# Kernel optimization log

Measured on AMD Instinct MI355X. Metric: run time of the kernel, lower is better.

Reference implementation:

```python
import jax, jax.numpy as jnp
import numpy as np

NUM = 5   # grid intervals
K = 3     # spline order


def make_grid(in_dim, num=NUM, k=K, lo=-1.0, hi=1.0):
    # pykan: linspace over [lo,hi] with num+1 knots, extended by k on each side
    g = np.linspace(lo, hi, num + 1)
    h = (g[-1] - g[0]) / num
    left = g[0] - h * np.arange(k, 0, -1)
    right = g[-1] + h * np.arange(1, k + 1)
    g = np.concatenate([left, g, right])  # (num + 2k + 1,)
    return jnp.asarray(np.broadcast_to(g, (in_dim, g.shape[0])), dtype=jnp.float32)


def b_batch(x, grid, k=K):
    # x: (B, in), grid: (in, G) -> B-spline bases (B, in, G-k-1) via Cox-de Boor
    xe = x[:, :, None]                      # (B, in, 1)
    g = grid[None]                          # (1, in, G)
    B = ((xe >= g[:, :, :-1]) & (xe < g[:, :, 1:])).astype(x.dtype)
    for ki in range(1, k + 1):
        B = ((xe - g[:, :, :-(ki + 1)]) / (g[:, :, ki:-1] - g[:, :, :-(ki + 1)]) * B[:, :, :-1]
             + (g[:, :, ki + 1:] - xe) / (g[:, :, ki + 1:] - g[:, :, 1:-ki]) * B[:, :, 1:])
    return jnp.nan_to_num(B)


def kan_layer(x, grid, coef, scale_base, scale_sp, mask, k=K):
    # x: (B, in); coef: (in, out, num+k); scales/mask: (in, out)
    base = jax.nn.silu(x)                             # (B, in)
    Bsp = b_batch(x, grid, k)                         # (B, in, num+k)
    y = jnp.einsum('bik,iok->bio', Bsp, coef)         # spline curves (B, in, out)
    y = scale_base[None] * base[:, :, None] + scale_sp[None] * y
    y = mask[None] * y
    return jnp.sum(y, axis=1)                         # (B, out)


def setup_inputs() -> dict:
    key = jax.random.key(0)
    ks = jax.random.split(key, 10)
    B, IN, HID, OUT = 4096, 1024, 256, 128
    KC = NUM + K  # coef count per edge
    x = jax.random.normal(ks[0], (B, IN), dtype=jnp.float32)
    W1 = jax.random.normal(ks[1], (HID, IN), dtype=jnp.float32) / np.sqrt(IN)
    b1 = jnp.zeros((HID,), dtype=jnp.float32)
    grid1 = make_grid(HID)
    coef1 = jax.random.normal(ks[2], (HID, HID, KC), dtype=jnp.float32) * 0.1
    sb1 = jax.random.normal(ks[3], (HID, HID), dtype=jnp.float32) / np.sqrt(HID)
    sp1 = jnp.ones((HID, HID), dtype=jnp.float32) / np.sqrt(HID)
    mask1 = jnp.ones((HID, HID), dtype=jnp.float32)
    grid2 = make_grid(HID)
    coef2 = jax.random.normal(ks[4], (HID, OUT, KC), dtype=jnp.float32) * 0.1
    sb2 = jax.random.normal(ks[5], (HID, OUT), dtype=jnp.float32) / np.sqrt(HID)
    sp2 = jnp.ones((HID, OUT), dtype=jnp.float32) / np.sqrt(HID)
    mask2 = jnp.ones((HID, OUT), dtype=jnp.float32)
    return {"x": x, "W1": W1, "b1": b1,
            "grid1": grid1, "coef1": coef1, "sb1": sb1, "sp1": sp1, "mask1": mask1,
            "grid2": grid2, "coef2": coef2, "sb2": sb2, "sp2": sp2, "mask2": mask2}


def reference(x, W1, b1, grid1, coef1, sb1, sp1, mask1, grid2, coef2, sb2, sp2, mask2):
    h = x @ W1.T + b1                                  # fc1
    h = kan_layer(h, grid1, coef1, sb1, sp1, mask1)    # kanl1
    out = kan_layer(h, grid2, coef2, sb2, sp2, mask2)  # kanl2
    return out
```

## Files before the change

kernel.cpp:

```cpp
#include <hip/hip_runtime.h>
#include <math.h>

typedef unsigned short u16;
typedef u16 u16x4 __attribute__((ext_vector_type(4)));
typedef u16 u16x8 __attribute__((ext_vector_type(8)));
typedef float f32x4 __attribute__((ext_vector_type(4)));
typedef float f32x16 __attribute__((ext_vector_type(16)));
typedef __bf16 bf16x8 __attribute__((ext_vector_type(8)));

#define KC 8
#define K2L 2304

__device__ __forceinline__ u16 f2bf_rne(float f) {
  unsigned u = __float_as_uint(f);
  u += 0x7FFFu + ((u >> 16) & 1u);
  return (u16)(u >> 16);
}
__device__ __forceinline__ float bf2f(u16 h) {
  return __uint_as_float(((unsigned)h) << 16);
}

__device__ __forceinline__ void gload16(const u16* g, u16* l) {
  __builtin_amdgcn_global_load_lds(
      (const __attribute__((address_space(1))) unsigned*)g,
      (__attribute__((address_space(3))) unsigned*)l, 16, 0, 0);
}
template <int N>
__device__ __forceinline__ void vmwait() {
  if constexpr (N == 0)      asm volatile("s_waitcnt vmcnt(0)" ::: "memory");
  else if constexpr (N == 3) asm volatile("s_waitcnt vmcnt(3)" ::: "memory");
  else if constexpr (N == 4) asm volatile("s_waitcnt vmcnt(4)" ::: "memory");
  else if constexpr (N == 6) asm volatile("s_waitcnt vmcnt(6)" ::: "memory");
  else if constexpr (N == 8) asm volatile("s_waitcnt vmcnt(8)" ::: "memory");
  else static_assert(N == 0, "unsupported vmcnt literal");
}

__device__ __forceinline__ void split4(const float* X, u16* hi, u16* lo, int i) {
  f32x4 v = ((const f32x4*)X)[i];
  u16x4 h, l;
#pragma unroll
  for (int c = 0; c < 4; ++c) {
    u16 hb = f2bf_rne(v[c]);
    h[c] = hb;
    l[c] = f2bf_rne(v[c] - bf2f(hb));
  }
  ((u16x4*)hi)[i] = h;
  ((u16x4*)lo)[i] = l;
}
__device__ __forceinline__ void split4hi(const float* X, u16* hi, int i) {
  f32x4 v = ((const f32x4*)X)[i];
  u16x4 h;
#pragma unroll
  for (int c = 0; c < 4; ++c) h[c] = f2bf_rne(v[c]);
  ((u16x4*)hi)[i] = h;
}
__device__ __forceinline__ void wc_one(const float* coef, const float* sb, const float* sp,
                                       const float* mask, u16* W, int N, int idx) {
  int o = idx / K2L;
  int r = idx - o * K2L;
  int i = r / 9;
  int c = r - i * 9;
  int io = i * N + o;
  float m = mask[io];
  float v = (c == 0) ? m * sb[io] : m * sp[io] * coef[(size_t)io * KC + (c - 1)];
  W[idx] = f2bf_rne(v);
}

__global__ void prep_kernel(const float* __restrict__ x, const float* __restrict__ W1,
                            const float* __restrict__ coef1, const float* __restrict__ sb1,
                            const float* __restrict__ sp1, const float* __restrict__ mask1,
                            const float* __restrict__ coef2, const float* __restrict__ sb2,
                            const float* __restrict__ sp2, const float* __restrict__ mask2,
                            u16* __restrict__ xs_hi,
                            u16* __restrict__ w1_hi, u16* __restrict__ w1_lo,
                            u16* __restrict__ wc1, u16* __restrict__ wc2) {
  const int b = blockIdx.x, tid = threadIdx.x;
  if (b < 4096) {
    split4hi(x, xs_hi, b * 256 + tid);
  } else if (b < 4096 + 256) {
    split4(W1, w1_hi, w1_lo, (b - 4096) * 256 + tid);
  } else if (b < 4096 + 256 + 2304) {
    wc_one(coef1, sb1, sp1, mask1, wc1, 256, (b - 4352) * 256 + tid);
  } else {
    wc_one(coef2, sb2, sp2, mask2, wc2, 128, (b - 6656) * 256 + tid);
  }
}

struct Spl {
  float g[12];
  float d1[11], d2[10], d3[9];
};
__device__ __forceinline__ void spl_init(const float* __restrict__ grid, Spl& sp) {
#pragma unroll
  for (int j = 0; j < 12; ++j) sp.g[j] = grid[j];
#pragma unroll
  for (int j = 0; j < 11; ++j) sp.d1[j] = 1.0f / (sp.g[j + 1] - sp.g[j]);
#pragma unroll
  for (int j = 0; j < 10; ++j) sp.d2[j] = 1.0f / (sp.g[j + 2] - sp.g[j]);
#pragma unroll
  for (int j = 0; j < 9; ++j) sp.d3[j] = 1.0f / (sp.g[j + 3] - sp.g[j]);
}
__device__ __forceinline__ void expand_one(float v, const Spl& sp, u16* dst) {
  float Bv[11];
#pragma unroll
  for (int j = 0; j < 11; ++j) Bv[j] = (v >= sp.g[j] && v < sp.g[j + 1]) ? 1.0f : 0.0f;
#pragma unroll
  for (int j = 0; j < 10; ++j)
    Bv[j] = (v - sp.g[j]) * sp.d1[j] * Bv[j] + (sp.g[j + 2] - v) * sp.d1[j + 1] * Bv[j + 1];
#pragma unroll
  for (int j = 0; j < 9; ++j)
    Bv[j] = (v - sp.g[j]) * sp.d2[j] * Bv[j] + (sp.g[j + 3] - v) * sp.d2[j + 1] * Bv[j + 1];
#pragma unroll
  for (int j = 0; j < 8; ++j)
    Bv[j] = (v - sp.g[j]) * sp.d3[j] * Bv[j] + (sp.g[j + 4] - v) * sp.d3[j + 1] * Bv[j + 1];
  dst[0] = f2bf_rne(v / (1.0f + __expf(-v)));
#pragma unroll
  for (int k = 0; k < 8; ++k) dst[1 + k] = f2bf_rne(Bv[k]);
}

template <int NREG, int MQ, int NQ, int KG, bool EXPAND>
__global__ __launch_bounds__(512) void gemmW(
    const u16* __restrict__ A0, const u16* __restrict__ B0, const u16* __restrict__ B1,
    const float* __restrict__ bias, const float* __restrict__ grid,
    void* __restrict__ outv, int M, int N, int K, int nsteps) {
  static_assert(MQ * NQ * KG == 8, "8 waves");
  constexpr int BM = MQ * 32, BN = NQ * 32;
  constexpr int ASZ = BM * 128;
  constexpr int BUF_U16 = (BM + BN) * 128;
  constexpr int NCH = (BM + BN) * 16;
  constexpr int LPT = NCH / 512;
  constexpr int SPK = 8 / KG;
  __shared__ __align__(16) u16 smu[4 * BUF_U16];

  const int tid = threadIdx.x;
  const int lane = tid & 63;
  const int wid = tid >> 6;
  const int q = wid % (MQ * NQ);
  const int kg = wid / (MQ * NQ);
  const int mq = (NQ == 2) ? (q >> 1) : q;
  const int nq = (NQ == 2) ? (q & 1) : 0;

  const int nb = N / BN;
  const int nwg = (M / BM) * nb;
  const int bid = blockIdx.x;
  const int swz = (bid & 7) * (nwg >> 3) + (bid >> 3);
  const int tm = (swz / nb) * BM;
  const int tn = (swz % nb) * BN;

  const u16* pA0 = A0 + (size_t)tm * K;
  const u16* pB0 = B0 + (size_t)tn * K;
  const u16* pB1 = (NREG == 2) ? B1 + (size_t)tn * K : nullptr;

  int srcO[LPT];
  bool isA[LPT];
#pragma unroll
  for (int k = 0; k < LPT; ++k) {
    int c = tid + k * 512;
    bool a = c < BM * 16;
    int r = a ? (c >> 4) : ((c - BM * 16) >> 4);
    int sl = c & 15;
    isA[k] = a;
    srcO[k] = r * K + (((sl ^ (r & 15)) & 15) << 3);
  }

  const int lr = lane & 31;
  const int khf = lane >> 5;

  int offA[SPK], offB[SPK];
#pragma unroll
  for (int s = 0; s < SPK; ++s) {
    int slice = kg * SPK + s;
    int rowA = mq * 32 + lr;
    int rowB = nq * 32 + lr;
    offA[s] = rowA * 128 + ((((slice * 2 + khf) ^ (rowA & 15)) & 15) << 3);
    offB[s] = rowB * 128 + ((((slice * 2 + khf) ^ (rowB & 15)) & 15) << 3);
  }

  auto stage = [&](int buf, int step) {
    int kk;
    const u16 *Ab, *Bb;
    if constexpr (NREG == 2) {
      int reg = step >> 3;
      kk = (step & 7) << 7;
      Ab = pA0;
      Bb = (reg == 1) ? pB1 : pB0;
    } else {
      kk = step << 7;
      Ab = pA0;
      Bb = pB0;
    }
    u16* sb = smu + buf * BUF_U16;
#pragma unroll
    for (int k = 0; k < LPT; ++k)
      gload16((isA[k] ? Ab : Bb) + srcO[k] + kk, sb + (k * 512 + wid * 64) * 8);
  };

  f32x16 acc0 = {}, acc1 = {};
  stage(0, 0);
  stage(1, 1);
  for (int i = 0; i < nsteps; ++i) {
    if (i + 2 < nsteps) {
      stage((i + 2) & 3, i + 2);
      vmwait<2 * LPT>();
    } else if (i + 1 < nsteps) {
      vmwait<LPT>();
    } else {
      vmwait<0>();
    }
    __builtin_amdgcn_sched_barrier(0);
    __builtin_amdgcn_s_barrier();
    __builtin_amdgcn_sched_barrier(0);

    const u16* sb = smu + (i & 3) * BUF_U16;
    bf16x8 af[SPK], bfr[SPK];
#pragma unroll
    for (int s = 0; s < SPK; ++s) {
      af[s] = *(const bf16x8*)(sb + offA[s]);
      bfr[s] = *(const bf16x8*)(sb + ASZ + offB[s]);
    }
#pragma unroll
    for (int s = 0; s < SPK; ++s) {
      f32x16& ac = (s & 1) ? acc1 : acc0;
      ac = __builtin_amdgcn_mfma_f32_32x32x16_bf16(af[s], bfr[s], ac, 0, 0, 0);
    }
  }
  f32x16 accv = acc0 + acc1;

  const int rbase = 4 * khf;
  const int rowq = mq * 32, colq = nq * 32;

  float* Fr = (float*)smu;
  if constexpr (KG == 2) {
    __syncthreads();
    if (kg == 1) {
#pragma unroll
      for (int r = 0; r < 16; ++r) {
        int row = rowq + rbase + (r & 3) + 8 * (r >> 2);
        Fr[row * BN + colq + lr] = accv[r];
      }
    }
    __syncthreads();
    if (kg == 0) {
#pragma unroll
      for (int r = 0; r < 16; ++r) {
        int row = rowq + rbase + (r & 3) + 8 * (r >> 2);
        accv[r] += Fr[row * BN + colq + lr];
      }
    }
  } else {
    __syncthreads();
    if (kg >= 2) {
#pragma unroll
      for (int r = 0; r < 16; ++r) {
        int row = rowq + rbase + (r & 3) + 8 * (r >> 2);
        Fr[(kg - 2) * (BM * BN) + row * BN + colq + lr] = accv[r];
      }
    }
    __syncthreads();
    if (kg < 2) {
#pragma unroll
      for (int r = 0; r < 16; ++r) {
        int row = rowq + rbase + (r & 3) + 8 * (r >> 2);
        accv[r] += Fr[kg * (BM * BN) + row * BN + colq + lr];
      }
    }
    __syncthreads();
    if (kg == 1) {
#pragma unroll
      for (int r = 0; r < 16; ++r) {
        int row = rowq + rbase + (r & 3) + 8 * (r >> 2);
        Fr[row * BN + colq + lr] = accv[r];
      }
    }
    __syncthreads();
    if (kg == 0) {
#pragma unroll
      for (int r = 0; r < 16; ++r) {
        int row = rowq + rbase + (r & 3) + 8 * (r >> 2);
        accv[r] += Fr[row * BN + colq + lr];
      }
    }
  }

  if constexpr (EXPAND) {
    Spl sp;
    spl_init(grid, sp);
    __syncthreads();
    u16* Fl = smu;
    if (kg == 0) {
      int col = colq + lr;
      float bv = bias ? bias[tn + col] : 0.0f;
#pragma unroll
      for (int r = 0; r < 16; ++r) {
        int row = rowq + rbase + (r & 3) + 8 * (r >> 2);
        expand_one(accv[r] + bv, sp, Fl + (size_t)row * (BN * 9) + col * 9);
      }
    }
    __syncthreads();
    u16* Fout = (u16*)outv;
    constexpr int RB = BN * 9 / 8;
    constexpr int CH = BM * RB;
    const size_t fstride = (size_t)N * 9;
    for (int ch = tid; ch < CH; ch += 512) {
      int r = ch / RB, o = ch - r * RB;
      *(u16x8*)(Fout + (size_t)(tm + r) * fstride + (size_t)tn * 9 + o * 8) =
          *(const u16x8*)(Fl + (size_t)ch * 8);
    }
  } else {
    if (kg == 0) {
      float* Cp = (float*)outv;
      const int cbase = tn + colq + lr;
#pragma unroll
      for (int r = 0; r < 16; ++r) {
        int row = tm + rowq + rbase + (r & 3) + 8 * (r >> 2);
        Cp[(size_t)row * N + cbase] = accv[r];
      }
    }
  }
}

extern "C" void kernel_launch(void* const* d_in, const int* in_sizes, int n_in,
                              void* d_out, int out_size, void* d_ws, size_t ws_size,
                              hipStream_t stream) {
  (void)in_sizes; (void)n_in; (void)out_size; (void)ws_size;
  const float* x     = (const float*)d_in[0];
  const float* W1    = (const float*)d_in[1];
  const float* b1    = (const float*)d_in[2];
  const float* grid1 = (const float*)d_in[3];
  const float* coef1 = (const float*)d_in[4];
  const float* sb1   = (const float*)d_in[5];
  const float* sp1   = (const float*)d_in[6];
  const float* mask1 = (const float*)d_in[7];
  const float* grid2 = (const float*)d_in[8];
  const float* coef2 = (const float*)d_in[9];
  const float* sb2   = (const float*)d_in[10];
  const float* sp2   = (const float*)d_in[11];
  const float* mask2 = (const float*)d_in[12];
  float* outp = (float*)d_out;

  char* ws = (char*)d_ws;
  size_t off = 0;
  auto alloc = [&](size_t bytes) {
    char* p = ws + off;
    off += (bytes + 255) & ~(size_t)255;
    return (void*)p;
  };
  u16* xs_hi  = (u16*)alloc((size_t)4096 * 1024 * 2);
  u16* w1_hi  = (u16*)alloc((size_t)256 * 1024 * 2);
  u16* w1_lo  = (u16*)alloc((size_t)256 * 1024 * 2);
  u16* wc1    = (u16*)alloc((size_t)256 * K2L * 2);
  u16* wc2    = (u16*)alloc((size_t)128 * K2L * 2);
  u16* F1     = (u16*)alloc((size_t)4096 * K2L * 2);
  u16* F2     = (u16*)alloc((size_t)4096 * K2L * 2);

  prep_kernel<<<7808, 256, 0, stream>>>(x, W1, coef1, sb1, sp1, mask1,
                                        coef2, sb2, sp2, mask2,
                                        xs_hi, w1_hi, w1_lo, wc1, wc2);

  gemmW<2, 2, 2, 2, true><<<256, 512, 0, stream>>>(
      xs_hi, w1_hi, w1_lo, b1, grid1, F1, 4096, 256, 1024, 16);

  gemmW<1, 2, 2, 2, true><<<256, 512, 0, stream>>>(
      F1, wc1, nullptr, nullptr, grid2, F2, 4096, 256, 2304, 18);

  gemmW<1, 2, 1, 4, false><<<256, 512, 0, stream>>>(
      F2, wc2, nullptr, nullptr, nullptr, outp, 4096, 128, 2304, 18);
}
```

Before: 62.06 us.

## Drop W1 low-part split and share spline expansion across both K-groups

Removes the bf16 hi/lo split of W1, so the first GEMM runs only 8 K-steps against a single bf16 copy of W1 instead of 16 steps over two copies. It also changes the KG=2 reduction to a symmetric exchange so both K-group waves hold the full sum. Each group then expands half of the rows into B-spline features, splitting work that one group did alone before. This lowers the accuracy of fc1, since W1 now carries only bf16 precision, which could affect tolerance near spline knot boundaries.

```diff
diff --git a/kernel.cpp b/kernel.cpp
--- a/kernel.cpp
+++ b/kernel.cpp
@@ -15,9 +15,6 @@
   unsigned u = __float_as_uint(f);
   u += 0x7FFFu + ((u >> 16) & 1u);
   return (u16)(u >> 16);
-}
-__device__ __forceinline__ float bf2f(u16 h) {
-  return __uint_as_float(((unsigned)h) << 16);
 }
 
 __device__ __forceinline__ void gload16(const u16* g, u16* l) {
@@ -35,18 +32,6 @@
   else static_assert(N == 0, "unsupported vmcnt literal");
 }
 
-__device__ __forceinline__ void split4(const float* X, u16* hi, u16* lo, int i) {
-  f32x4 v = ((const f32x4*)X)[i];
-  u16x4 h, l;
-#pragma unroll
-  for (int c = 0; c < 4; ++c) {
-    u16 hb = f2bf_rne(v[c]);
-    h[c] = hb;
-    l[c] = f2bf_rne(v[c] - bf2f(hb));
-  }
-  ((u16x4*)hi)[i] = h;
-  ((u16x4*)lo)[i] = l;
-}
 __device__ __forceinline__ void split4hi(const float* X, u16* hi, int i) {
   f32x4 v = ((const f32x4*)X)[i];
   u16x4 h;
@@ -71,14 +56,13 @@
                             const float* __restrict__ sp1, const float* __restrict__ mask1,
                             const float* __restrict__ coef2, const float* __restrict__ sb2,
                             const float* __restrict__ sp2, const float* __restrict__ mask2,
-                            u16* __restrict__ xs_hi,
-                            u16* __restrict__ w1_hi, u16* __restrict__ w1_lo,
+                            u16* __restrict__ xs_hi, u16* __restrict__ w1_hi,
                             u16* __restrict__ wc1, u16* __restrict__ wc2) {
   const int b = blockIdx.x, tid = threadIdx.x;
   if (b < 4096) {
     split4hi(x, xs_hi, b * 256 + tid);
   } else if (b < 4096 + 256) {
-    split4(W1, w1_hi, w1_lo, (b - 4096) * 256 + tid);
+    split4hi(W1, w1_hi, (b - 4096) * 256 + tid);
   } else if (b < 4096 + 256 + 2304) {
     wc_one(coef1, sb1, sp1, mask1, wc1, 256, (b - 4352) * 256 + tid);
   } else {
@@ -118,17 +102,16 @@
   for (int k = 0; k < 8; ++k) dst[1 + k] = f2bf_rne(Bv[k]);
 }
 
-template <int NREG, int MQ, int NQ, int KG, bool EXPAND>
+template <int MQ, int NQ, int KG, bool EXPAND>
 __global__ __launch_bounds__(512) void gemmW(
-    const u16* __restrict__ A0, const u16* __restrict__ B0, const u16* __restrict__ B1,
+    const u16* __restrict__ A0, const u16* __restrict__ B0,
     const float* __restrict__ bias, const float* __restrict__ grid,
     void* __restrict__ outv, int M, int N, int K, int nsteps) {
   static_assert(MQ * NQ * KG == 8, "8 waves");
   constexpr int BM = MQ * 32, BN = NQ * 32;
   constexpr int ASZ = BM * 128;
   constexpr int BUF_U16 = (BM + BN) * 128;
-  constexpr int NCH = (BM + BN) * 16;
-  constexpr int LPT = NCH / 512;
+  constexpr int LPT = (BM + BN) * 16 / 512;
   constexpr int SPK = 8 / KG;
   __shared__ __align__(16) u16 smu[4 * BUF_U16];
 
@@ -149,7 +132,6 @@
 
   const u16* pA0 = A0 + (size_t)tm * K;
   const u16* pB0 = B0 + (size_t)tn * K;
-  const u16* pB1 = (NREG == 2) ? B1 + (size_t)tn * K : nullptr;
 
   int srcO[LPT];
   bool isA[LPT];
@@ -177,22 +159,11 @@
   }
 
   auto stage = [&](int buf, int step) {
-    int kk;
-    const u16 *Ab, *Bb;
-    if constexpr (NREG == 2) {
-      int reg = step >> 3;
-      kk = (step & 7) << 7;
-      Ab = pA0;
-      Bb = (reg == 1) ? pB1 : pB0;
-    } else {
-      kk = step << 7;
-      Ab = pA0;
-      Bb = pB0;
-    }
+    int kk = step << 7;
     u16* sb = smu + buf * BUF_U16;
 #pragma unroll
     for (int k = 0; k < LPT; ++k)
-      gload16((isA[k] ? Ab : Bb) + srcO[k] + kk, sb + (k * 512 + wid * 64) * 8);
+      gload16((isA[k] ? pA0 : pB0) + srcO[k] + kk, sb + (k * 512 + wid * 64) * 8);
   };
 
   f32x16 acc0 = {}, acc1 = {};
@@ -232,20 +203,16 @@
   float* Fr = (float*)smu;
   if constexpr (KG == 2) {
     __syncthreads();
-    if (kg == 1) {
-#pragma unroll
-      for (int r = 0; r < 16; ++r) {
-        int row = rowq + rbase + (r & 3) + 8 * (r >> 2);
-        Fr[row * BN + colq + lr] = accv[r];
-      }
-    }
-    __syncthreads();
-    if (kg == 0) {
-#pragma unroll
-      for (int r = 0; r < 16; ++r) {
-        int row = rowq + rbase + (r & 3) + 8 * (r >> 2);
-        accv[r] += Fr[row * BN + colq + lr];
-      }
+#pragma unroll
+    for (int r = 0; r < 16; ++r) {
+      int row = rowq + rbase + (r & 3) + 8 * (r >> 2);
+      Fr[kg * (BM * BN) + row * BN + colq + lr] = accv[r];
+    }
+    __syncthreads();
+#pragma unroll
+    for (int r = 0; r < 16; ++r) {
+      int row = rowq + rbase + (r & 3) + 8 * (r >> 2);
+      accv[r] += Fr[(1 - kg) * (BM * BN) + row * BN + colq + lr];
     }
   } else {
     __syncthreads();
@@ -287,13 +254,16 @@
     spl_init(grid, sp);
     __syncthreads();
     u16* Fl = smu;
-    if (kg == 0) {
+    {
       int col = colq + lr;
       float bv = bias ? bias[tn + col] : 0.0f;
-#pragma unroll
-      for (int r = 0; r < 16; ++r) {
-        int row = rowq + rbase + (r & 3) + 8 * (r >> 2);
-        expand_one(accv[r] + bv, sp, Fl + (size_t)row * (BN * 9) + col * 9);
+      const int r0 = kg * 8, r1 = r0 + 8;
+#pragma unroll
+      for (int r = 0; r < 16; ++r) {
+        if (r >= r0 && r < r1) {
+          int row = rowq + rbase + (r & 3) + 8 * (r >> 2);
+          expand_one(accv[r] + bv, sp, Fl + (size_t)row * (BN * 9) + col * 9);
+        }
       }
     }
     __syncthreads();
@@ -347,7 +317,6 @@
   };
   u16* xs_hi  = (u16*)alloc((size_t)4096 * 1024 * 2);
   u16* w1_hi  = (u16*)alloc((size_t)256 * 1024 * 2);
-  u16* w1_lo  = (u16*)alloc((size_t)256 * 1024 * 2);
   u16* wc1    = (u16*)alloc((size_t)256 * K2L * 2);
   u16* wc2    = (u16*)alloc((size_t)128 * K2L * 2);
   u16* F1     = (u16*)alloc((size_t)4096 * K2L * 2);
@@ -355,14 +324,14 @@
 
   prep_kernel<<<7808, 256, 0, stream>>>(x, W1, coef1, sb1, sp1, mask1,
                                         coef2, sb2, sp2, mask2,
-                                        xs_hi, w1_hi, w1_lo, wc1, wc2);
-
-  gemmW<2, 2, 2, 2, true><<<256, 512, 0, stream>>>(
-      xs_hi, w1_hi, w1_lo, b1, grid1, F1, 4096, 256, 1024, 16);
-
-  gemmW<1, 2, 2, 2, true><<<256, 512, 0, stream>>>(
-      F1, wc1, nullptr, nullptr, grid2, F2, 4096, 256, 2304, 18);
-
-  gemmW<1, 2, 1, 4, false><<<256, 512, 0, stream>>>(
-      F2, wc2, nullptr, nullptr, nullptr, outp, 4096, 128, 2304, 18);
-}
+                                        xs_hi, w1_hi, wc1, wc2);
+
+  gemmW<2, 2, 2, true><<<256, 512, 0, stream>>>(
+      xs_hi, w1_hi, b1, grid1, F1, 4096, 256, 1024, 8);
+
+  gemmW<2, 2, 2, true><<<256, 512, 0, stream>>>(
+      F1, wc1, nullptr, grid2, F2, 4096, 256, 2304, 18);
+
+  gemmW<2, 1, 4, false><<<256, 512, 0, stream>>>(
+      F2, wc2, nullptr, nullptr, outp, 4096, 128, 2304, 18);
+}
```

New measurement: 57.46 us, median of 2. 1.08x faster.
